# Optimization experiments

Measured on AMD Instinct MI355X. Metric: run time of the kernel, lower is better.

Reference implementation:

```python
import jax, jax.numpy as jnp
import numpy as np

N_NODES = 32768
N_EDGES = 196608
N_GRAPHS = 256
DEG = 6
HID = 128
RVD = 16
EMB = HID - RVD   # atom/bond embedding dim = hidden - random_vec_dim
VOCAB = 128
TGT = 256
DEPTH = 5
N_AGG = 4         # mean, max, min, std
N_SC = 3          # identity, amplification, attenuation
EPS = 1e-5


def setup_inputs() -> dict:
    key = jax.random.key(0)
    ks = jax.random.split(key, 12)

    def g(i, shape, scale=0.05):
        return jax.random.normal(ks[i], shape, dtype=jnp.float32) * scale

    return {
        "atom_feats": jax.random.randint(ks[0], (N_NODES, 9), 0, 100),
        "bond_feats": jax.random.randint(ks[1], (N_EDGES, 3), 0, 4),
        "src": jax.random.randint(ks[2], (N_EDGES,), 0, N_NODES),
        # every node receives exactly DEG messages (DGL reduce requires in-edges)
        "dst": jnp.repeat(jnp.arange(N_NODES), DEG),
        "graph_ids": jnp.repeat(jnp.arange(N_GRAPHS), N_NODES // N_GRAPHS),
        "n_graphs": N_GRAPHS,
        "rand_x": jax.random.normal(ks[3], (N_NODES, RVD), dtype=jnp.float32),   # std=1.0
        "rand_edge": jax.random.normal(ks[4], (N_EDGES, RVD), dtype=jnp.float32),
        "atom_emb": g(5, (9, VOCAB, EMB)),
        "bond_emb": g(6, (3, VOCAB, EMB)),
        "pre_W": g(7, (DEPTH, 3 * HID, HID)),
        "pre_b": jnp.zeros((DEPTH, HID), jnp.float32),
        "post_W": g(8, (DEPTH, (N_AGG * N_SC + 1) * HID, HID)),
        "post_b": jnp.zeros((DEPTH, HID), jnp.float32),
        "ro_W1": g(9, (3 * HID, HID)),
        "ro_b1": jnp.zeros((HID,), jnp.float32),
        "ro_W2": g(10, (HID, TGT)),
        "ro_b2": jnp.zeros((TGT,), jnp.float32),
    }


def reference(atom_feats, bond_feats, src, dst, graph_ids, n_graphs,
              rand_x, rand_edge, atom_emb, bond_emb,
              pre_W, pre_b, post_W, post_b, ro_W1, ro_b1, ro_W2, ro_b2):
    n = atom_feats.shape[0]
    # OGB-style encoders: sum of per-column embeddings, then concat random vec
    h = jnp.concatenate([atom_emb[jnp.arange(9), atom_feats].sum(1), rand_x], -1)   # [N, HID]
    ef = jnp.concatenate([bond_emb[jnp.arange(3), bond_feats].sum(1), rand_edge], -1)  # [E, HID]

    deg = jax.ops.segment_sum(jnp.ones((dst.shape[0],), h.dtype), dst, n)
    degc = jnp.maximum(deg, 1.0)[:, None]
    logD = jnp.log(deg + 1.0)[:, None]                 # avg_d['log'] = 1.0
    inv_logD = jnp.where(logD > 0, 1.0 / jnp.maximum(logD, EPS), 0.0)

    def layer(hc, p):
        pW, pb, qW, qb = p
        # pretrans MLP on [src_feat, dst_feat, edge_feat]; last_activation = activation (relu)
        z = jnp.concatenate([hc[src], hc[dst], ef], -1)          # [E, 3*HID]
        e = jax.nn.relu(z @ pW + pb)                             # [E, HID]
        s = jax.ops.segment_sum(e, dst, n)
        mean = s / degc
        mean_sq = jax.ops.segment_sum(e * e, dst, n) / degc
        mx = jax.ops.segment_max(e, dst, n)
        mn = jax.ops.segment_min(e, dst, n)
        std = jnp.sqrt(jax.nn.relu(mean_sq - mean * mean) + EPS)
        agg = jnp.concatenate([mean, mx, mn, std], -1)           # [N, 4*HID]
        scaled = jnp.concatenate([agg, agg * logD, agg * inv_logD], -1)  # [N, 12*HID]
        h_new = jnp.concatenate([hc, scaled], -1) @ qW + qb + hc  # posttrans (linear) + residual
        return h_new, None

    h, _ = jax.lax.scan(layer, h, (pre_W, pre_b, post_W, post_b))

    # multi-aggregator readout: mean, sum, max per graph
    cnt = jnp.maximum(jax.ops.segment_sum(jnp.ones((n,), h.dtype), graph_ids, n_graphs), 1.0)[:, None]
    gsum = jax.ops.segment_sum(h, graph_ids, n_graphs)
    gmax = jax.ops.segment_max(h, graph_ids, n_graphs)
    r = jnp.concatenate([gsum / cnt, gsum, gmax], -1)            # [G, 3*HID]
    return jax.nn.relu(r @ ro_W1 + ro_b1) @ ro_W2 + ro_b2        # [G, TGT]
```

## Files before the change

### kernel.cpp

```cpp
#include <hip/hip_runtime.h>
#include <hip/hip_bf16.h>

#define N_NODES 32768
#define N_EDGES 196608
#define N_GRAPHS 256
#define DEG 6
#define HID 128
#define RVD 16
#define EMB 112
#define VOCAB 128
#define TGT 256
#define DEPTH 5

#define LOG7 1.9459101090932196f
#define ILOG7 0.5138983423697507f

typedef __hip_bfloat16 bf16;
using frag_ab = __attribute__((ext_vector_type(8))) short;
using frag_cd = __attribute__((ext_vector_type(4))) float;
typedef float f32x2 __attribute__((ext_vector_type(2)));

static __device__ __forceinline__ float b2f(bf16 x) { return __bfloat162float(x); }
static __device__ __forceinline__ bf16  f2b(float x) { return __float2bfloat16(x); }
static __device__ __forceinline__ float us2f(unsigned short u) {
    unsigned int x = ((unsigned int)u) << 16;
    return __uint_as_float(x);
}
static __device__ __forceinline__ unsigned short f2us(float x) {
    bf16 b = __float2bfloat16(x);
    return *reinterpret_cast<unsigned short*>(&b);
}

#define PB_ENC  16384
#define PB_WB   (PB_ENC + 640)
#define PB_WC   (PB_WB + 1600)
#define PB_WR   (PB_WC + 80)
#define PB_CODE (PB_WR + 768)
#define PB_T    (PB_CODE + 320)

__global__ __launch_bounds__(256) void prep_k(const int* __restrict__ af, const float* __restrict__ rx,
                                              const float* __restrict__ aemb, bf16* __restrict__ h,
                                              const float* __restrict__ preW, const float* __restrict__ preB,
                                              const float* __restrict__ postW,
                                              const int* __restrict__ bfeat, const float* __restrict__ bemb,
                                              bf16* __restrict__ wb, bf16* __restrict__ wc,
                                              bf16* __restrict__ wrB, unsigned char* __restrict__ codeA,
                                              bf16* __restrict__ Tb) {
    int blk = blockIdx.x, tid = threadIdx.x;
    if (blk < PB_ENC) {
        int v = blk * 2 + (tid >> 7), c = tid & 127;
        float val;
        if (c < EMB) {
            val = 0.f;
            #pragma unroll
            for (int i = 0; i < 9; ++i) {
                int f = af[v * 9 + i];
                val += aemb[(i * VOCAB + f) * EMB + c];
            }
        } else {
            val = rx[v * RVD + (c - EMB)];
        }
        h[(size_t)v * HID + c] = f2b(val);
    } else if (blk < PB_WB) {
        int idx = (blk - PB_ENC) * 256 + tid;
        if (idx < DEPTH * 32768) {
            int j = idx & 7, L = (idx >> 3) & 63, nt = (idx >> 9) & 15, ks = (idx >> 13) & 3, l = idx >> 15;
            int k = ks * 32 + ((L >> 4) * 8) + j;
            int n = nt * 16 + (L & 15);
            const float* W = preW + (size_t)l * 384 * 128;
            float v = (n < 128) ? W[k * 128 + n] : W[(128 + k) * 128 + (n - 128)];
            wb[idx] = f2b(v);
        }
    } else if (blk < PB_WC) {
        int idx = (blk - PB_WB) * 256 + tid;
        if (idx < DEPTH * 81920) {
            int j = idx & 7, L = (idx >> 3) & 63, nt = (idx >> 9) & 7;
            int t = idx >> 12;
            int ks = t % 20, l = t / 20;
            int k = ks * 32 + ((L >> 4) * 8) + j;
            int n = nt * 16 + (L & 15);
            const float* W = postW + (size_t)l * 1664 * 128;
            float v;
            if (k < 128) {
                v = W[k * 128 + n];
            } else {
                int jj = k - 128;
                v = W[(128 + jj) * 128 + n] + LOG7 * W[(640 + jj) * 128 + n] + ILOG7 * W[(1152 + jj) * 128 + n];
            }
            wc[idx] = f2b(v);
        }
    } else if (blk < PB_WR) {
        int idx = (blk - PB_WC) * 256 + tid;
        if (idx < DEPTH * 4096) {
            int j = idx & 7, L = (idx >> 3) & 63, nt = (idx >> 9) & 7, l = idx >> 12;
            int k = ((L >> 4) * 8) + j;
            int n = nt * 16 + (L & 15);
            float v = (k < 16) ? preW[(size_t)l * 384 * 128 + (368 + k) * 128 + n] : 0.f;
            wrB[idx] = f2b(v);
        }
    } else if (blk < PB_CODE) {
        int e = (blk - PB_WR) * 256 + tid;
        if (e < N_EDGES)
            codeA[e] = (unsigned char)(bfeat[e * 3] | (bfeat[e * 3 + 1] << 2) | (bfeat[e * 3 + 2] << 4));
    } else {
        if (tid < 128) {
            int t = blk - PB_CODE;
            int l = t >> 6, cd = t & 63, c = tid;
            int f0 = cd & 3, f1 = (cd >> 2) & 3, f2 = cd >> 4;
            const float* W = preW + (size_t)l * 384 * 128 + 256 * 128;
            float acc = preB[l * 128 + c];
            #pragma unroll 4
            for (int k = 0; k < EMB; ++k) {
                float bsk = bemb[(0 * VOCAB + f0) * EMB + k]
                          + bemb[(1 * VOCAB + f1) * EMB + k]
                          + bemb[(2 * VOCAB + f2) * EMB + k];
                acc += bsk * W[k * 128 + c];
            }
            Tb[(size_t)(l * 64 + cd) * 128 + c] = f2b(acc);
        }
    }
}

__global__ __launch_bounds__(256) void gemm_z12(const bf16* __restrict__ A,
                                                const bf16* __restrict__ Bp,
                                                bf16* __restrict__ C) {
    int lane = threadIdx.x & 63;
    int wave = threadIdx.x >> 6;
    int m = lane & 15, quad = lane >> 4;
    int row0 = blockIdx.x * 64 + wave * 16;

    frag_cd acc[16];
    #pragma unroll
    for (int nt = 0; nt < 16; ++nt)
        #pragma unroll
        for (int i = 0; i < 4; ++i) acc[nt][i] = 0.f;

    const frag_ab* Bf = (const frag_ab*)Bp;
    const bf16* arow = A + (size_t)(row0 + m) * 128;
    #pragma unroll
    for (int ks = 0; ks < 4; ++ks) {
        frag_ab a = *(const frag_ab*)(arow + ks * 32 + quad * 8);
        #pragma unroll
        for (int nt = 0; nt < 16; ++nt) {
            frag_ab b = Bf[(ks * 16 + nt) * 64 + lane];
            acc[nt] = __builtin_amdgcn_mfma_f32_16x16x32_bf16(a, b, acc[nt], 0, 0, 0);
        }
    }
    #pragma unroll
    for (int nt = 0; nt < 16; ++nt) {
        int col = nt * 16 + m;
        #pragma unroll
        for (int r = 0; r < 4; ++r) {
            int row = row0 + quad * 4 + r;
            C[(size_t)row * 256 + col] = f2b(acc[nt][r]);
        }
    }
}

__global__ __launch_bounds__(256, 4) void fused_layer(bf16* __restrict__ h,
                                                      const bf16* __restrict__ Zcur,
                                                      const int* __restrict__ src,
                                                      const unsigned char* __restrict__ code,
                                                      const float* __restrict__ rand_edge,
                                                      const bf16* __restrict__ Tb,
                                                      const float* __restrict__ Wr,
                                                      const bf16* __restrict__ Bp,
                                                      const float* __restrict__ bias,
                                                      const bf16* __restrict__ Bn,
                                                      bf16* __restrict__ Znext) {
    __shared__ __align__(16) bf16 agg_lds[32 * 520];
    __shared__ __align__(16) float relds[4][384];

    int tid = threadIdx.x;
    int lane = tid & 63, wave = tid >> 6;
    int ml = lane & 15, quad = lane >> 4;
    int row0 = blockIdx.x * 32;

    const unsigned short* Zu = (const unsigned short*)Zcur;
    const unsigned short* Tu = (const unsigned short*)Tb;
    unsigned short* Ag = (unsigned short*)agg_lds;
    int c = lane * 2;

    {
        const int vbase = row0 + wave * 8;

        f32x2 wr2[16];
        #pragma unroll
        for (int k = 0; k < 16; ++k) {
            float2 w2 = *(const float2*)(Wr + k * 128 + c);
            wr2[k].x = w2.x; wr2[k].y = w2.y;
        }

        {
            const float2* rb = (const float2*)(rand_edge + (size_t)vbase * 96);
            float2 a0 = rb[lane], a1 = rb[lane + 64], a2 = rb[lane + 128];
            float2* rl = (float2*)relds[wave];
            rl[lane] = a0; rl[lane + 64] = a1; rl[lane + 128] = a2;
        }
        float2 rh0, rh1, rh2;

        int svs[2][6]; int cds[2][6];
        ushort2 z1u[2][6], tvu[2][6], z2u[2];

        {
            const int2* sp = (const int2*)(src + vbase * 6);
            int2 a = sp[0], b = sp[1], d = sp[2];
            svs[0][0] = a.x; svs[0][1] = a.y; svs[0][2] = b.x;
            svs[0][3] = b.y; svs[0][4] = d.x; svs[0][5] = d.y;
            const unsigned short* cp = (const unsigned short*)(code + vbase * 6);
            unsigned short x = cp[0], y = cp[1], z = cp[2];
            cds[0][0] = x & 255; cds[0][1] = x >> 8; cds[0][2] = y & 255;
            cds[0][3] = y >> 8;  cds[0][4] = z & 255; cds[0][5] = z >> 8;
        }
        z2u[0] = *(const ushort2*)(Zu + (size_t)vbase * 256 + 128 + c);
        #pragma unroll
        for (int j = 0; j < 6; ++j) z1u[0][j] = *(const ushort2*)(Zu + (size_t)svs[0][j] * 256 + c);
        #pragma unroll
        for (int j = 0; j < 6; ++j) tvu[0][j] = *(const ushort2*)(Tu + cds[0][j] * 128 + c);
        {
            const int2* sp = (const int2*)(src + (vbase + 1) * 6);
            int2 a = sp[0], b = sp[1], d = sp[2];
            svs[1][0] = a.x; svs[1][1] = a.y; svs[1][2] = b.x;
            svs[1][3] = b.y; svs[1][4] = d.x; svs[1][5] = d.y;
            const unsigned short* cp = (const unsigned short*)(code + (vbase + 1) * 6);
            unsigned short x = cp[0], y = cp[1], z = cp[2];
            cds[1][0] = x & 255; cds[1][1] = x >> 8; cds[1][2] = y & 255;
            cds[1][3] = y >> 8;  cds[1][4] = z & 255; cds[1][5] = z >> 8;
        }

        #pragma unroll
        for (int i = 0; i < 8; ++i) {
            const int s = i & 1, t = s ^ 1;
            if (i == 2) {
                const float2* rb2 = (const float2*)(rand_edge + (size_t)(vbase + 4) * 96);
                rh0 = rb2[lane]; rh1 = rb2[lane + 64]; rh2 = rb2[lane + 128];
            }
            if (i == 4) {
                float2* rl = (float2*)relds[wave];
                rl[lane] = rh0; rl[lane + 64] = rh1; rl[lane + 128] = rh2;
            }
            if (i < 7) {
                z2u[t] = *(const ushort2*)(Zu + (size_t)(vbase + i + 1) * 256 + 128 + c);
                #pragma unroll
                for (int j = 0; j < 6; ++j) z1u[t][j] = *(const ushort2*)(Zu + (size_t)svs[t][j] * 256 + c);
                #pragma unroll
                for (int j = 0; j < 6; ++j) tvu[t][j] = *(const ushort2*)(Tu + cds[t][j] * 128 + c);
            }
            if (i < 6) {
                const int2* sp = (const int2*)(src + (vbase + i + 2) * 6);
                int2 a = sp[0], b = sp[1], d = sp[2];
                svs[s][0] = a.x; svs[s][1] = a.y; svs[s][2] = b.x;
                svs[s][3] = b.y; svs[s][4] = d.x; svs[s][5] = d.y;
                const unsigned short* cp = (const unsigned short*)(code + (vbase + i + 2) * 6);
                unsigned short x = cp[0], y = cp[1], z = cp[2];
                cds[s][0] = x & 255; cds[s][1] = x >> 8; cds[s][2] = y & 255;
                cds[s][3] = y >> 8;  cds[s][4] = z & 255; cds[s][5] = z >> 8;
            }

            float z2a = us2f(z2u[s].x), z2b = us2f(z2u[s].y);
            f32x2 s2  = {0.f, 0.f}, ss2 = {0.f, 0.f};
            f32x2 mx2 = {-1e30f, -1e30f}, mn2 = {1e30f, 1e30f};
            #pragma unroll
            for (int j = 0; j < 6; ++j) {
                const float4* rp = (const float4*)&relds[wave][(i & 3) * 96 + j * 16];
                float4 r0 = rp[0], r1 = rp[1], r2 = rp[2], r3 = rp[3];
                f32x2 v2;
                v2.x = us2f(z1u[s][j].x) + z2a + us2f(tvu[s][j].x);
                v2.y = us2f(z1u[s][j].y) + z2b + us2f(tvu[s][j].y);
                float rk[16] = {r0.x, r0.y, r0.z, r0.w, r1.x, r1.y, r1.z, r1.w,
                                r2.x, r2.y, r2.z, r2.w, r3.x, r3.y, r3.z, r3.w};
                #pragma unroll
                for (int k = 0; k < 16; ++k) v2 += rk[k] * wr2[k];
                v2 = __builtin_elementwise_max(v2, (f32x2){0.f, 0.f});
                s2 += v2;
                ss2 += v2 * v2;
                mx2 = __builtin_elementwise_max(mx2, v2);
                mn2 = __builtin_elementwise_min(mn2, v2);
            }
            f32x2 mean2 = s2 * (1.f / 6.f);
            f32x2 msq2  = ss2 * (1.f / 6.f);
            f32x2 var2  = __builtin_elementwise_max(msq2 - mean2 * mean2, (f32x2){0.f, 0.f});
            float sda = sqrtf(var2.x + 1e-5f), sdb = sqrtf(var2.y + 1e-5f);
            int lrow = wave * 8 + i;
            size_t base = (size_t)lrow * 520 + c;
            *(ushort2*)(Ag + base)       = make_ushort2(f2us(mean2.x), f2us(mean2.y));
            *(ushort2*)(Ag + base + 128) = make_ushort2(f2us(mx2.x),   f2us(mx2.y));
            *(ushort2*)(Ag + base + 256) = make_ushort2(f2us(mn2.x),   f2us(mn2.y));
            *(ushort2*)(Ag + base + 384) = make_ushort2(f2us(sda),     f2us(sdb));
        }
    }
    __syncthreads();

    int ng = wave;

    frag_cd acc[2][2];
    #pragma unroll
    for (int m2 = 0; m2 < 2; ++m2)
        #pragma unroll
        for (int nt = 0; nt < 2; ++nt)
            #pragma unroll
            for (int i = 0; i < 4; ++i) acc[m2][nt][i] = 0.f;

    const frag_ab* Bf = (const frag_ab*)Bp;
    #pragma unroll
    for (int ks = 0; ks < 4; ++ks) {
        frag_ab b0 = Bf[(ks * 8 + ng * 2 + 0) * 64 + lane];
        frag_ab b1 = Bf[(ks * 8 + ng * 2 + 1) * 64 + lane];
        #pragma unroll
        for (int m2 = 0; m2 < 2; ++m2) {
            frag_ab a = *(const frag_ab*)(h + (size_t)(row0 + m2 * 16 + ml) * 128 + ks * 32 + quad * 8);
            acc[m2][0] = __builtin_amdgcn_mfma_f32_16x16x32_bf16(a, b0, acc[m2][0], 0, 0, 0);
            acc[m2][1] = __builtin_amdgcn_mfma_f32_16x16x32_bf16(a, b1, acc[m2][1], 0, 0, 0);
        }
    }
    #pragma unroll
    for (int ks = 0; ks < 16; ++ks) {
        frag_ab b0 = Bf[((4 + ks) * 8 + ng * 2 + 0) * 64 + lane];
        frag_ab b1 = Bf[((4 + ks) * 8 + ng * 2 + 1) * 64 + lane];
        #pragma unroll
        for (int m2 = 0; m2 < 2; ++m2) {
            frag_ab a = *(const frag_ab*)(agg_lds + (size_t)(m2 * 16 + ml) * 520 + ks * 32 + quad * 8);
            acc[m2][0] = __builtin_amdgcn_mfma_f32_16x16x32_bf16(a, b0, acc[m2][0], 0, 0, 0);
            acc[m2][1] = __builtin_amdgcn_mfma_f32_16x16x32_bf16(a, b1, acc[m2][1], 0, 0, 0);
        }
    }

    __syncthreads();

    float* pgemm = (float*)agg_lds;
    #pragma unroll
    for (int nt = 0; nt < 2; ++nt) {
        int col = (ng * 2 + nt) * 16 + ml;
        float bs_ = bias[col];
        #pragma unroll
        for (int m2 = 0; m2 < 2; ++m2) {
            #pragma unroll
            for (int r2 = 0; r2 < 4; ++r2) {
                int lr = m2 * 16 + quad * 4 + r2;
                pgemm[lr * 132 + col] = acc[m2][nt][r2] + bs_;
            }
        }
    }
    __syncthreads();

    bf16* newh = agg_lds + 8448;
    {
        int row = tid >> 3, cg = tid & 7;
        const float4* pg = (const float4*)(pgemm + row * 132 + cg * 16);
        float4 p0 = pg[0], p1 = pg[1], p2 = pg[2], p3 = pg[3];
        unsigned short* hrow = (unsigned short*)(h + (size_t)(row0 + row) * 128 + cg * 16);
        frag_ab h0 = *(const frag_ab*)hrow;
        frag_ab h1 = *(const frag_ab*)(hrow + 8);
        float nv[16] = {p0.x, p0.y, p0.z, p0.w, p1.x, p1.y, p1.z, p1.w,
                        p2.x, p2.y, p2.z, p2.w, p3.x, p3.y, p3.z, p3.w};
        #pragma unroll
        for (int j = 0; j < 8; ++j) nv[j]     += us2f((unsigned short)h0[j]);
        #pragma unroll
        for (int j = 0; j < 8; ++j) nv[8 + j] += us2f((unsigned short)h1[j]);
        frag_ab o0, o1;
        #pragma unroll
        for (int j = 0; j < 8; ++j) o0[j] = (short)f2us(nv[j]);
        #pragma unroll
        for (int j = 0; j < 8; ++j) o1[j] = (short)f2us(nv[8 + j]);
        *(frag_ab*)hrow = o0;
        *(frag_ab*)(hrow + 8) = o1;
        *(frag_ab*)&newh[row * 136 + cg * 16] = o0;
        *(frag_ab*)&newh[row * 136 + cg * 16 + 8] = o1;
    }

    if (Bn) {
        __syncthreads();
        const frag_ab* Bf2 = (const frag_ab*)Bn;
        frag_cd a2[2][4];
        #pragma unroll
        for (int m2 = 0; m2 < 2; ++m2)
            #pragma unroll
            for (int nt = 0; nt < 4; ++nt)
                #pragma unroll
                for (int i = 0; i < 4; ++i) a2[m2][nt][i] = 0.f;
        #pragma unroll
        for (int ks = 0; ks < 4; ++ks) {
            frag_ab bb[4];
            #pragma unroll
            for (int nt = 0; nt < 4; ++nt)
                bb[nt] = Bf2[(ks * 16 + ng * 4 + nt) * 64 + lane];
            #pragma unroll
            for (int m2 = 0; m2 < 2; ++m2) {
                frag_ab a = *(const frag_ab*)&newh[(m2 * 16 + ml) * 136 + ks * 32 + quad * 8];
                #pragma unroll
                for (int nt = 0; nt < 4; ++nt)
                    a2[m2][nt] = __builtin_amdgcn_mfma_f32_16x16x32_bf16(a, bb[nt], a2[m2][nt], 0, 0, 0);
            }
        }
        bf16* ztile = agg_lds;
        #pragma unroll
        for (int m2 = 0; m2 < 2; ++m2) {
            #pragma unroll
            for (int nt = 0; nt < 4; ++nt) {
                int col = (ng * 4 + nt) * 16 + ml;
                #pragma unroll
                for (int r2 = 0; r2 < 4; ++r2) {
                    int lr = m2 * 16 + quad * 4 + r2;
                    ztile[lr * 264 + col] = f2b(a2[m2][nt][r2]);
                }
            }
        }
        __syncthreads();
        int row = tid >> 3, cg = tid & 7;
        unsigned short* zr = (unsigned short*)(Znext + (size_t)(row0 + row) * 256 + cg * 32);
        const unsigned short* zs = (const unsigned short*)ztile + row * 264 + cg * 32;
        #pragma unroll
        for (int k2 = 0; k2 < 4; ++k2)
            *(frag_ab*)(zr + k2 * 8) = *(const frag_ab*)(zs + k2 * 8);
    }
}

__global__ __launch_bounds__(128) void readout(const bf16* __restrict__ h, const float* __restrict__ W1,
                                               const float* __restrict__ b1, const float* __restrict__ W2,
                                               const float* __restrict__ b2, float* __restrict__ out) {
    __shared__ float r[384];
    __shared__ float y1[128];
    int g = blockIdx.x, c = threadIdx.x;
    float s = 0.f, mx = -1e30f;
    for (int v = 0; v < 128; ++v) {
        float hv = b2f(h[((size_t)g * 128 + v) * HID + c]);
        s += hv; mx = fmaxf(mx, hv);
    }
    r[c] = s * (1.f / 128.f);
    r[128 + c] = s;
    r[256 + c] = mx;
    __syncthreads();
    float a1 = b1[c];
    for (int k = 0; k < 384; ++k) a1 += r[k] * W1[k * 128 + c];
    y1[c] = fmaxf(a1, 0.f);
    __syncthreads();
    #pragma unroll
    for (int o = 0; o < 2; ++o) {
        int t = c + o * 128;
        float a2 = b2[t];
        for (int k = 0; k < 128; ++k) a2 += y1[k] * W2[k * 256 + t];
        out[(size_t)g * 256 + t] = a2;
    }
}

extern "C" void kernel_launch(void* const* d_in, const int* in_sizes, int n_in,
                              void* d_out, int out_size, void* d_ws, size_t ws_size,
                              hipStream_t stream) {
    const int*   atom_feats = (const int*)d_in[0];
    const int*   bond_feats = (const int*)d_in[1];
    const int*   src        = (const int*)d_in[2];
    const float* rand_x     = (const float*)d_in[6];
    const float* rand_edge  = (const float*)d_in[7];
    const float* atom_emb   = (const float*)d_in[8];
    const float* bond_emb   = (const float*)d_in[9];
    const float* pre_W      = (const float*)d_in[10];
    const float* pre_b      = (const float*)d_in[11];
    const float* post_W     = (const float*)d_in[12];
    const float* post_b     = (const float*)d_in[13];
    const float* ro_W1      = (const float*)d_in[14];
    const float* ro_b1      = (const float*)d_in[15];
    const float* ro_W2      = (const float*)d_in[16];
    const float* ro_b2      = (const float*)d_in[17];

    char* p = (char*)d_ws;
    auto alloc = [&](size_t bytes) {
        char* r = p;
        p += (bytes + 255) & ~(size_t)255;
        return r;
    };
    bf16*  h    = (bf16*) alloc((size_t)N_NODES * HID * 2);
    bf16*  z12a = (bf16*) alloc((size_t)N_NODES * 256 * 2);
    bf16*  z12b = (bf16*) alloc((size_t)N_NODES * 256 * 2);
    bf16*  wb   = (bf16*) alloc((size_t)DEPTH * 32768 * 2);
    bf16*  wc   = (bf16*) alloc((size_t)DEPTH * 81920 * 2);
    bf16*  wrB  = (bf16*) alloc((size_t)DEPTH * 4096 * 2);
    bf16*  Tb   = (bf16*) alloc((size_t)DEPTH * 64 * 128 * 2);
    unsigned char* code = (unsigned char*)alloc(N_EDGES);

    prep_k<<<PB_T, 256, 0, stream>>>(atom_feats, rand_x, atom_emb, h,
                                     pre_W, pre_b, post_W,
                                     bond_feats, bond_emb,
                                     wb, wc, wrB, code, Tb);

    gemm_z12<<<N_NODES / 64, 256, 0, stream>>>(h, wb, z12a);

    bf16* zc = z12a;
    bf16* zn = z12b;
    for (int l = 0; l < DEPTH; ++l) {
        const bf16* wbn = (l + 1 < DEPTH) ? (wb + (size_t)(l + 1) * 32768) : nullptr;
        fused_layer<<<N_NODES / 32, 256, 0, stream>>>(
            h, zc, src, code, rand_edge,
            Tb + (size_t)l * 8192,
            pre_W + (size_t)l * 384 * 128 + 368 * 128,
            wc + (size_t)l * 81920,
            post_b + l * HID,
            wbn, zn);
        bf16* t = zc; zc = zn; zn = t;
    }

    readout<<<N_GRAPHS, 128, 0, stream>>>(h, ro_W1, ro_b1, ro_W2, ro_b2, (float*)d_out);
}
```

Measured before the change: 322.7 us.

## Compute random-edge projection with MFMA instead of scalar FMA loop

Replaces the per-lane 16-term scalar FMA dot product of rand_edge against the pre_W random-vector slice with a bf16 MFMA (16x16x32), run once per pair of nodes (12 edges). The result goes to per-wave LDS as bf16 and is read back during aggregation. The launch-bounds occupancy hint drops from 4 to 3 blocks. This removes the register-resident fp32 weight slice and many VALU FMAs, but adds bf16 rounding of rand_edge and of the projection, extra LDS traffic, and relies on the prebuilt wrB fragment layout.

Result: slower. 338.2 us (+4.8%).

```diff
diff --git a/kernel.cpp b/kernel.cpp
--- a/kernel.cpp
+++ b/kernel.cpp
@@ -22,6 +22,10 @@
 
 static __device__ __forceinline__ float b2f(bf16 x) { return __bfloat162float(x); }
 static __device__ __forceinline__ bf16  f2b(float x) { return __float2bfloat16(x); }
+static __device__ __forceinline__ short f2s(float x) {
+    bf16 b = __float2bfloat16(x);
+    return *reinterpret_cast<short*>(&b);
+}
 static __device__ __forceinline__ float us2f(unsigned short u) {
     unsigned int x = ((unsigned int)u) << 16;
     return __uint_as_float(x);
@@ -157,19 +161,19 @@
     }
 }
 
-__global__ __launch_bounds__(256, 4) void fused_layer(bf16* __restrict__ h,
+__global__ __launch_bounds__(256, 3) void fused_layer(bf16* __restrict__ h,
                                                       const bf16* __restrict__ Zcur,
                                                       const int* __restrict__ src,
                                                       const unsigned char* __restrict__ code,
                                                       const float* __restrict__ rand_edge,
                                                       const bf16* __restrict__ Tb,
-                                                      const float* __restrict__ Wr,
+                                                      const bf16* __restrict__ WrB,
                                                       const bf16* __restrict__ Bp,
                                                       const float* __restrict__ bias,
                                                       const bf16* __restrict__ Bn,
                                                       bf16* __restrict__ Znext) {
     __shared__ __align__(16) bf16 agg_lds[32 * 520];
-    __shared__ __align__(16) float relds[4][384];
+    __shared__ __align__(16) bf16 rdot_lds[4][16 * 136];
 
     int tid = threadIdx.x;
     int lane = tid & 63, wave = tid >> 6;
@@ -183,21 +187,9 @@
 
     {
         const int vbase = row0 + wave * 8;
-
-        f32x2 wr2[16];
-        #pragma unroll
-        for (int k = 0; k < 16; ++k) {
-            float2 w2 = *(const float2*)(Wr + k * 128 + c);
-            wr2[k].x = w2.x; wr2[k].y = w2.y;
-        }
-
-        {
-            const float2* rb = (const float2*)(rand_edge + (size_t)vbase * 96);
-            float2 a0 = rb[lane], a1 = rb[lane + 64], a2 = rb[lane + 128];
-            float2* rl = (float2*)relds[wave];
-            rl[lane] = a0; rl[lane + 64] = a1; rl[lane + 128] = a2;
-        }
-        float2 rh0, rh1, rh2;
+        bf16* rdw = &rdot_lds[wave][0];
+        const unsigned short* rdu = (const unsigned short*)rdw;
+        const frag_ab* BfR = (const frag_ab*)WrB;
 
         int svs[2][6]; int cds[2][6];
         ushort2 z1u[2][6], tvu[2][6], z2u[2];
@@ -231,14 +223,32 @@
         #pragma unroll
         for (int i = 0; i < 8; ++i) {
             const int s = i & 1, t = s ^ 1;
-            if (i == 2) {
-                const float2* rb2 = (const float2*)(rand_edge + (size_t)(vbase + 4) * 96);
-                rh0 = rb2[lane]; rh1 = rb2[lane + 64]; rh2 = rb2[lane + 128];
-            }
-            if (i == 4) {
-                float2* rl = (float2*)relds[wave];
-                rl[lane] = rh0; rl[lane + 64] = rh1; rl[lane + 128] = rh2;
-            }
+
+            if ((i & 1) == 0) {
+                int ebase = (vbase + i) * 6;
+                frag_ab a;
+                if (quad < 2) {
+                    int me = (ml < 12) ? ml : 11;
+                    const float4* rp = (const float4*)(rand_edge + (size_t)(ebase + me) * 16 + quad * 8);
+                    float4 A = rp[0], B = rp[1];
+                    a[0] = f2s(A.x); a[1] = f2s(A.y); a[2] = f2s(A.z); a[3] = f2s(A.w);
+                    a[4] = f2s(B.x); a[5] = f2s(B.y); a[6] = f2s(B.z); a[7] = f2s(B.w);
+                } else {
+                    #pragma unroll
+                    for (int j = 0; j < 8; ++j) a[j] = 0;
+                }
+                #pragma unroll
+                for (int nt = 0; nt < 8; ++nt) {
+                    frag_cd acc4;
+                    #pragma unroll
+                    for (int q = 0; q < 4; ++q) acc4[q] = 0.f;
+                    acc4 = __builtin_amdgcn_mfma_f32_16x16x32_bf16(a, BfR[nt * 64 + lane], acc4, 0, 0, 0);
+                    #pragma unroll
+                    for (int r = 0; r < 4; ++r)
+                        rdw[(quad * 4 + r) * 136 + nt * 16 + ml] = f2b(acc4[r]);
+                }
+            }
+
             if (i < 7) {
                 z2u[t] = *(const ushort2*)(Zu + (size_t)(vbase + i + 1) * 256 + 128 + c);
                 #pragma unroll
@@ -257,20 +267,20 @@
                 cds[s][3] = y >> 8;  cds[s][4] = z & 255; cds[s][5] = z >> 8;
             }
 
+            ushort2 rdv[6];
+            {
+                const unsigned short* rb = rdu + ((i & 1) * 6) * 136 + c;
+                #pragma unroll
+                for (int j = 0; j < 6; ++j) rdv[j] = *(const ushort2*)(rb + j * 136);
+            }
             float z2a = us2f(z2u[s].x), z2b = us2f(z2u[s].y);
             f32x2 s2  = {0.f, 0.f}, ss2 = {0.f, 0.f};
             f32x2 mx2 = {-1e30f, -1e30f}, mn2 = {1e30f, 1e30f};
             #pragma unroll
             for (int j = 0; j < 6; ++j) {
-                const float4* rp = (const float4*)&relds[wave][(i & 3) * 96 + j * 16];
-                float4 r0 = rp[0], r1 = rp[1], r2 = rp[2], r3 = rp[3];
                 f32x2 v2;
-                v2.x = us2f(z1u[s][j].x) + z2a + us2f(tvu[s][j].x);
-                v2.y = us2f(z1u[s][j].y) + z2b + us2f(tvu[s][j].y);
-                float rk[16] = {r0.x, r0.y, r0.z, r0.w, r1.x, r1.y, r1.z, r1.w,
-                                r2.x, r2.y, r2.z, r2.w, r3.x, r3.y, r3.z, r3.w};
-                #pragma unroll
-                for (int k = 0; k < 16; ++k) v2 += rk[k] * wr2[k];
+                v2.x = us2f(z1u[s][j].x) + z2a + us2f(tvu[s][j].x) + us2f(rdv[j].x);
+                v2.y = us2f(z1u[s][j].y) + z2b + us2f(tvu[s][j].y) + us2f(rdv[j].y);
                 v2 = __builtin_elementwise_max(v2, (f32x2){0.f, 0.f});
                 s2 += v2;
                 ss2 += v2 * v2;
@@ -491,7 +501,7 @@
         fused_layer<<<N_NODES / 32, 256, 0, stream>>>(
             h, zc, src, code, rand_edge,
             Tb + (size_t)l * 8192,
-            pre_W + (size_t)l * 384 * 128 + 368 * 128,
+            wrB + (size_t)l * 4096,
             wc + (size_t)l * 81920,
             post_b + l * HID,
             wbn, zn);
```
